# Kernel optimization log

Measured on AMD Instinct MI355X. Metric: run time of the kernel, lower is better.

## Reference

```python
import jax, jax.numpy as jnp
import numpy as np

N_NODES = 100000


def _glorot(key, shape):
    fan_in, fan_out = shape[1], shape[0]
    lim = np.sqrt(6.0 / (fan_in + fan_out))
    return jax.random.uniform(key, shape, jnp.float32, -lim, lim)


def setup_inputs() -> dict:
    key = jax.random.key(0)
    ks = jax.random.split(key, 12)
    x = jax.random.normal(ks[0], (N_NODES, 64), jnp.float32)
    edge_index = jax.random.randint(ks[1], (2, 1600000), 0, N_NODES, jnp.int64)
    return {
        "x": x,
        "edge_index": edge_index,
        # SAGEConv layer 1: lin_l (neighbors, with bias), lin_r (root, no bias)
        "W1l": _glorot(ks[2], (64, 64)), "b1": jnp.zeros((64,), jnp.float32), "W1r": _glorot(ks[3], (64, 64)),
        "W2l": _glorot(ks[4], (64, 64)), "b2": jnp.zeros((64,), jnp.float32), "W2r": _glorot(ks[5], (64, 64)),
        "W3l": _glorot(ks[6], (32, 64)), "b3": jnp.zeros((32,), jnp.float32), "W3r": _glorot(ks[7], (32, 64)),
        "Wreg": _glorot(ks[8], (1, 32)), "breg": jnp.zeros((1,), jnp.float32),
    }


def _sage_conv(x, src, dst, Wl, b, Wr):
    # mean aggregation of source-node features at destination nodes
    msg_sum = jax.ops.segment_sum(x[src], dst, num_segments=N_NODES)  # [N, d]
    deg = jax.ops.segment_sum(jnp.ones_like(src, dtype=x.dtype), dst, num_segments=N_NODES)
    mean = msg_sum / jnp.maximum(deg, 1.0)[:, None]
    return mean @ Wl.T + b + x @ Wr.T


def reference(x, edge_index, W1l, b1, W1r, W2l, b2, W2r, W3l, b3, W3r, Wreg, breg):
    src, dst = edge_index[0], edge_index[1]
    h = jax.nn.relu(_sage_conv(x, src, dst, W1l, b1, W1r))
    h = jax.nn.relu(_sage_conv(h, src, dst, W2l, b2, W2r))
    h = jax.nn.relu(_sage_conv(h, src, dst, W3l, b3, W3r))
    return (h @ Wreg.T + breg).squeeze(-1)  # [N]
```

## Files before the change

kernel.cpp:

```cpp
#include <hip/hip_runtime.h>
#include <math.h>

#define N_NODES 100000
#define N_EDGES 1600000
#define NB 782
#define NTILES 6250
#define NPART 256

typedef unsigned int uint;
typedef __attribute__((ext_vector_type(8))) short bf16x8;
typedef __attribute__((ext_vector_type(4))) float f32x4;

__device__ inline ushort f2bf(float f) {
    uint u = __float_as_uint(f);
    uint r = (u + 0x7fffu + ((u >> 16) & 1u)) >> 16;
    return (ushort)r;
}
__device__ inline uint pack2bf(float lo, float hi) {
    return (uint)f2bf(lo) | ((uint)f2bf(hi) << 16);
}

__global__ void misc_kernel(const float* __restrict__ W1l, const float* __restrict__ W1r,
                            const float* __restrict__ W2l, const float* __restrict__ W2r,
                            const float* __restrict__ W3l, const float* __restrict__ W3r,
                            ushort* __restrict__ wf,
                            const float* __restrict__ x, ushort* __restrict__ xb) {
    if (blockIdx.x < 80) {
        int idx = blockIdx.x * 256 + threadIdx.x;
        if (idx >= 20480) return;
        const float *Wl, *Wr;
        int base, KT;
        if (idx < 8192)       { base = 0;     Wl = W1l; Wr = W1r; KT = 128; }
        else if (idx < 16384) { base = 8192;  Wl = W2l; Wr = W2r; KT = 128; }
        else if (idx < 18432) { base = 16384; Wl = W3l; Wr = 0;   KT = 64; }
        else                  { base = 18432; Wl = W3r; Wr = 0;   KT = 64; }
        int r = idx - base;
        int f = r >> 9;
        int l = (r >> 3) & 63;
        int i = r & 7;
        int nks = KT >> 5;
        int nt = f / nks, ks = f - nt * nks;
        int k = ks * 32 + ((l >> 4) << 3) + i;
        int j = nt * 16 + (l & 15);
        float v = (k < 64) ? Wl[j * 64 + k] : Wr[j * 64 + (k - 64)];
        wf[idx] = f2bf(v);
    } else {
        const int n4 = N_NODES * 64 / 4;
        int i0 = (blockIdx.x - 80) * 256 + threadIdx.x;
        for (int i = i0; i < n4; i += 400 * 256) {
            float4 v = ((const float4*)x)[i];
            uint2 o;
            o.x = pack2bf(v.x, v.y);
            o.y = pack2bf(v.z, v.w);
            ((uint2*)xb)[i] = o;
        }
    }
}

__global__ void bucket_hist(const int* __restrict__ dst, int* __restrict__ hist2D, int nE) {
    __shared__ int hist[NB];
    const int PER = (N_EDGES + NPART - 1) / NPART;
    int e0 = blockIdx.x * PER;
    int e1 = min(e0 + PER, nE);
    for (int i = threadIdx.x; i < NB; i += 1024) hist[i] = 0;
    __syncthreads();
    for (int e = e0 + threadIdx.x; e < e1; e += 1024)
        atomicAdd(&hist[dst[e] >> 7], 1);
    __syncthreads();
    for (int i = threadIdx.x; i < NB; i += 1024)
        hist2D[blockIdx.x * NB + i] = hist[i];
}

__global__ void scan_buckets(const int* __restrict__ hist2D, int* __restrict__ bucketBase,
                             int* __restrict__ base2D) {
    __shared__ int s[1024];
    int tid = threadIdx.x;
    int tot = 0;
    if (tid < NB)
        for (int b = 0; b < NPART; ++b) tot += hist2D[b * NB + tid];
    s[tid] = tot;
    __syncthreads();
    for (int off = 1; off < 1024; off <<= 1) {
        int t = (tid >= off) ? s[tid - off] : 0;
        __syncthreads();
        s[tid] += t;
        __syncthreads();
    }
    if (tid < NB) {
        int run = s[tid] - tot;
        bucketBase[tid] = run;
        for (int b = 0; b < NPART; ++b) {
            base2D[b * NB + tid] = run;
            run += hist2D[b * NB + tid];
        }
    }
    if (tid == 0) bucketBase[NB] = s[NB - 1];
}

__global__ void partition_kernel(const int* __restrict__ src, const int* __restrict__ dst,
                                 const int* __restrict__ base2D, int* __restrict__ part, int nE) {
    __shared__ int base[NB];
    __shared__ int rank[NB];
    const int PER = (N_EDGES + NPART - 1) / NPART;
    int e0 = blockIdx.x * PER;
    int e1 = min(e0 + PER, nE);
    for (int i = threadIdx.x; i < NB; i += 1024) {
        base[i] = base2D[blockIdx.x * NB + i];
        rank[i] = 0;
    }
    __syncthreads();
    for (int e = e0 + threadIdx.x; e < e1; e += 1024) {
        int d = dst[e];
        int bk = d >> 7;
        int r = atomicAdd(&rank[bk], 1);
        part[base[bk] + r] = src[e] | ((d & 127) << 20);
    }
}

__global__ void bucket_fill2(const int* __restrict__ bucketBase, const int* __restrict__ part,
                             int* __restrict__ col, int* __restrict__ rowptr,
                             float* __restrict__ invdeg, int n) {
    __shared__ int cnt[128];
    __shared__ int cnt2[128];
    __shared__ int exclS[128];
    __shared__ int s[128];
    int b = blockIdx.x;
    int d0 = b << 7;
    int dl = min(128, n - d0);
    int ebeg = bucketBase[b], eend = bucketBase[b + 1];
    if (threadIdx.x < 128) { cnt[threadIdx.x] = 0; cnt2[threadIdx.x] = 0; }
    __syncthreads();
    for (int i = ebeg + (int)threadIdx.x; i < eend; i += 512)
        atomicAdd(&cnt[part[i] >> 20], 1);
    __syncthreads();
    if (threadIdx.x < 128) s[threadIdx.x] = cnt[threadIdx.x];
    __syncthreads();
    for (int off = 1; off < 128; off <<= 1) {
        int t = 0;
        if (threadIdx.x < 128 && threadIdx.x >= (unsigned)off) t = s[threadIdx.x - off];
        __syncthreads();
        if (threadIdx.x < 128) s[threadIdx.x] += t;
        __syncthreads();
    }
    if ((int)threadIdx.x < dl) {
        int c = cnt[threadIdx.x];
        int ex = ebeg + s[threadIdx.x] - c;
        rowptr[d0 + threadIdx.x] = ex;
        invdeg[d0 + threadIdx.x] = 1.0f / fmaxf((float)c, 1.0f);
        exclS[threadIdx.x] = ex;
    }
    if (threadIdx.x == 0 && d0 + dl == n) rowptr[n] = eend;
    __syncthreads();
    for (int i = ebeg + (int)threadIdx.x; i < eend; i += 512) {
        int v = part[i];
        int doff = v >> 20;
        int pos = exclS[doff] + atomicAdd(&cnt2[doff], 1);
        col[pos] = v & 0xFFFFF;
    }
}

__global__ void gather_mean(const ushort* __restrict__ xb, const int* __restrict__ rowptr,
                            const int* __restrict__ col, const float* __restrict__ invdeg,
                            ushort* __restrict__ meanb, int n) {
    int tid = blockIdx.x * blockDim.x + threadIdx.x;
    int wid = tid >> 6;
    int lane = threadIdx.x & 63;
    int grp = lane >> 3;
    int li = lane & 7;
    int node = wid * 8 + grp;
    if (node >= n) return;
    int beg = rowptr[node];
    int end = rowptr[node + 1];
    int fb = li * 8;
    float a0 = 0.f, a1 = 0.f, a2 = 0.f, a3 = 0.f, a4 = 0.f, a5 = 0.f, a6 = 0.f, a7 = 0.f;
    for (int i = beg; i < end; i += 8) {
        int idx = i + li;
        int ci = (idx < end) ? col[idx] : 0;
        int cnt = end - i;
#pragma unroll
        for (int t = 0; t < 8; ++t) {
            if (t < cnt) {
                int s = __shfl(ci, grp * 8 + t, 64);
                uint4 w = *(const uint4*)(xb + (size_t)s * 64 + fb);
                a0 += __uint_as_float(w.x << 16);
                a1 += __uint_as_float(w.x & 0xffff0000u);
                a2 += __uint_as_float(w.y << 16);
                a3 += __uint_as_float(w.y & 0xffff0000u);
                a4 += __uint_as_float(w.z << 16);
                a5 += __uint_as_float(w.z & 0xffff0000u);
                a6 += __uint_as_float(w.w << 16);
                a7 += __uint_as_float(w.w & 0xffff0000u);
            }
        }
    }
    float id = invdeg[node];
    uint4 o;
    o.x = pack2bf(a0 * id, a1 * id);
    o.y = pack2bf(a2 * id, a3 * id);
    o.z = pack2bf(a4 * id, a5 * id);
    o.w = pack2bf(a6 * id, a7 * id);
    *(uint4*)(meanb + (size_t)node * 64 + fb) = o;
}

__global__ void gather_mean32(const ushort* __restrict__ gb, const int* __restrict__ rowptr,
                              const int* __restrict__ col, const float* __restrict__ invdeg,
                              ushort* __restrict__ mean32b, int n) {
    int tid = blockIdx.x * blockDim.x + threadIdx.x;
    int wid = tid >> 6;
    int lane = threadIdx.x & 63;
    int grp = lane >> 2;
    int li = lane & 3;
    int node = wid * 16 + grp;
    if (node >= n) return;
    int beg = rowptr[node];
    int end = rowptr[node + 1];
    int fb = li * 8;
    float a0 = 0.f, a1 = 0.f, a2 = 0.f, a3 = 0.f, a4 = 0.f, a5 = 0.f, a6 = 0.f, a7 = 0.f;
    for (int i = beg; i < end; i += 4) {
        int idx = i + li;
        int ci = (idx < end) ? col[idx] : 0;
        int cnt = end - i;
#pragma unroll
        for (int t = 0; t < 4; ++t) {
            if (t < cnt) {
                int s = __shfl(ci, grp * 4 + t, 64);
                uint4 w = *(const uint4*)(gb + (size_t)s * 32 + fb);
                a0 += __uint_as_float(w.x << 16);
                a1 += __uint_as_float(w.x & 0xffff0000u);
                a2 += __uint_as_float(w.y << 16);
                a3 += __uint_as_float(w.y & 0xffff0000u);
                a4 += __uint_as_float(w.z << 16);
                a5 += __uint_as_float(w.z & 0xffff0000u);
                a6 += __uint_as_float(w.w << 16);
                a7 += __uint_as_float(w.w & 0xffff0000u);
            }
        }
    }
    float id = invdeg[node];
    uint4 o;
    o.x = pack2bf(a0 * id, a1 * id);
    o.y = pack2bf(a2 * id, a3 * id);
    o.z = pack2bf(a4 * id, a5 * id);
    o.w = pack2bf(a6 * id, a7 * id);
    *(uint4*)(mean32b + (size_t)node * 32 + fb) = o;
}

__global__ void __launch_bounds__(256)
mfma_transform(const ushort* __restrict__ rootb, const ushort* __restrict__ meanb,
               const ushort* __restrict__ wfrag, const float* __restrict__ bias,
               ushort* __restrict__ outb, int ntiles) {
    int wave = threadIdx.x >> 6;
    int lane = threadIdx.x & 63;

    bf16x8 wf[4][4];
#pragma unroll
    for (int nt = 0; nt < 4; ++nt)
#pragma unroll
        for (int ks = 0; ks < 4; ++ks)
            wf[nt][ks] = *(const bf16x8*)(wfrag + (size_t)((nt * 4 + ks) * 64 + lane) * 8);

    float bl[4];
#pragma unroll
    for (int nt = 0; nt < 4; ++nt) bl[nt] = bias[nt * 16 + (lane & 15)];

    int arow = lane & 15;
    int koff = (lane >> 4) * 8;
    int crow = (lane >> 4) * 4;
    int nwaves = gridDim.x * 4;

    for (int tile = blockIdx.x * 4 + wave; tile < ntiles; tile += nwaves) {
        int n0 = tile * 16;
        const ushort* mrow = meanb + (size_t)(n0 + arow) * 64 + koff;
        const ushort* xrow = rootb + (size_t)(n0 + arow) * 64 + koff;
        bf16x8 a0 = *(const bf16x8*)(mrow);
        bf16x8 a1 = *(const bf16x8*)(mrow + 32);
        bf16x8 a2 = *(const bf16x8*)(xrow);
        bf16x8 a3 = *(const bf16x8*)(xrow + 32);
#pragma unroll
        for (int nt = 0; nt < 4; ++nt) {
            f32x4 c = {0.f, 0.f, 0.f, 0.f};
            c = __builtin_amdgcn_mfma_f32_16x16x32_bf16(a0, wf[nt][0], c, 0, 0, 0);
            c = __builtin_amdgcn_mfma_f32_16x16x32_bf16(a1, wf[nt][1], c, 0, 0, 0);
            c = __builtin_amdgcn_mfma_f32_16x16x32_bf16(a2, wf[nt][2], c, 0, 0, 0);
            c = __builtin_amdgcn_mfma_f32_16x16x32_bf16(a3, wf[nt][3], c, 0, 0, 0);
#pragma unroll
            for (int i = 0; i < 4; ++i) {
                float v = fmaxf(c[i] + bl[nt], 0.0f);
                outb[(size_t)(n0 + crow + i) * 64 + nt * 16 + (lane & 15)] = f2bf(v);
            }
        }
    }
}

__global__ void __launch_bounds__(256)
mfma_pretrans3(const ushort* __restrict__ hb, const ushort* __restrict__ wfrag,
               ushort* __restrict__ gb, int ntiles) {
    int wave = threadIdx.x >> 6;
    int lane = threadIdx.x & 63;

    bf16x8 wf[2][2];
#pragma unroll
    for (int nt = 0; nt < 2; ++nt)
#pragma unroll
        for (int ks = 0; ks < 2; ++ks)
            wf[nt][ks] = *(const bf16x8*)(wfrag + (size_t)((nt * 2 + ks) * 64 + lane) * 8);

    int arow = lane & 15;
    int koff = (lane >> 4) * 8;
    int crow = (lane >> 4) * 4;
    int nwaves = gridDim.x * 4;

    for (int tile = blockIdx.x * 4 + wave; tile < ntiles; tile += nwaves) {
        int n0 = tile * 16;
        const ushort* hrow = hb + (size_t)(n0 + arow) * 64 + koff;
        bf16x8 a0 = *(const bf16x8*)(hrow);
        bf16x8 a1 = *(const bf16x8*)(hrow + 32);
#pragma unroll
        for (int nt = 0; nt < 2; ++nt) {
            f32x4 c = {0.f, 0.f, 0.f, 0.f};
            c = __builtin_amdgcn_mfma_f32_16x16x32_bf16(a0, wf[nt][0], c, 0, 0, 0);
            c = __builtin_amdgcn_mfma_f32_16x16x32_bf16(a1, wf[nt][1], c, 0, 0, 0);
#pragma unroll
            for (int i = 0; i < 4; ++i)
                gb[(size_t)(n0 + crow + i) * 32 + nt * 16 + (lane & 15)] = f2bf(c[i]);
        }
    }
}

__global__ void __launch_bounds__(256)
mfma_t3(const ushort* __restrict__ hb, const ushort* __restrict__ mean32b,
        const ushort* __restrict__ wfrag, const float* __restrict__ b3,
        const float* __restrict__ Wreg, const float* __restrict__ breg,
        float* __restrict__ out, int ntiles) {
    int wave = threadIdx.x >> 6;
    int lane = threadIdx.x & 63;

    bf16x8 wf[2][2];
#pragma unroll
    for (int nt = 0; nt < 2; ++nt)
#pragma unroll
        for (int ks = 0; ks < 2; ++ks)
            wf[nt][ks] = *(const bf16x8*)(wfrag + (size_t)((nt * 2 + ks) * 64 + lane) * 8);

    float bl[2], wr[2];
#pragma unroll
    for (int nt = 0; nt < 2; ++nt) {
        bl[nt] = b3[nt * 16 + (lane & 15)];
        wr[nt] = Wreg[nt * 16 + (lane & 15)];
    }
    float br = breg[0];

    int arow = lane & 15;
    int koff = (lane >> 4) * 8;
    int crow = (lane >> 4) * 4;
    int nwaves = gridDim.x * 4;

    for (int tile = blockIdx.x * 4 + wave; tile < ntiles; tile += nwaves) {
        int n0 = tile * 16;
        const ushort* hrow = hb + (size_t)(n0 + arow) * 64 + koff;
        bf16x8 a0 = *(const bf16x8*)(hrow);
        bf16x8 a1 = *(const bf16x8*)(hrow + 32);
        float part0 = 0.f, part1 = 0.f, part2 = 0.f, part3 = 0.f;
#pragma unroll
        for (int nt = 0; nt < 2; ++nt) {
            f32x4 c = {0.f, 0.f, 0.f, 0.f};
            c = __builtin_amdgcn_mfma_f32_16x16x32_bf16(a0, wf[nt][0], c, 0, 0, 0);
            c = __builtin_amdgcn_mfma_f32_16x16x32_bf16(a1, wf[nt][1], c, 0, 0, 0);
#pragma unroll
            for (int i = 0; i < 4; ++i) {
                ushort mw = mean32b[(size_t)(n0 + crow + i) * 32 + nt * 16 + (lane & 15)];
                float m = __uint_as_float((uint)mw << 16);
                float v = fmaxf(c[i] + bl[nt] + m, 0.0f) * wr[nt];
                if (i == 0) part0 += v;
                else if (i == 1) part1 += v;
                else if (i == 2) part2 += v;
                else part3 += v;
            }
        }
#pragma unroll
        for (int s = 1; s < 16; s <<= 1) {
            part0 += __shfl_xor(part0, s, 64);
            part1 += __shfl_xor(part1, s, 64);
            part2 += __shfl_xor(part2, s, 64);
            part3 += __shfl_xor(part3, s, 64);
        }
        if ((lane & 15) == 0) {
            float4 o;
            o.x = part0 + br; o.y = part1 + br; o.z = part2 + br; o.w = part3 + br;
            *(float4*)(out + n0 + crow) = o;
        }
    }
}

extern "C" void kernel_launch(void* const* d_in, const int* in_sizes, int n_in,
                              void* d_out, int out_size, void* d_ws, size_t ws_size,
                              hipStream_t stream) {
    const float* x    = (const float*)d_in[0];
    const int*   ei   = (const int*)d_in[1];
    const float* W1l  = (const float*)d_in[2];
    const float* b1   = (const float*)d_in[3];
    const float* W1r  = (const float*)d_in[4];
    const float* W2l  = (const float*)d_in[5];
    const float* b2   = (const float*)d_in[6];
    const float* W2r  = (const float*)d_in[7];
    const float* W3l  = (const float*)d_in[8];
    const float* b3   = (const float*)d_in[9];
    const float* W3r  = (const float*)d_in[10];
    const float* Wreg = (const float*)d_in[11];
    const float* breg = (const float*)d_in[12];

    const int* src = ei;
    const int* dst = ei + N_EDGES;

    char* p = (char*)d_ws;
    auto alloc = [&](size_t bytes) {
        char* r = p;
        p += (bytes + 255) & ~(size_t)255;
        return r;
    };
    int*    hist2D    = (int*)alloc((size_t)NPART * NB * sizeof(int));
    int*    base2D    = (int*)alloc((size_t)NPART * NB * sizeof(int));
    int*    bucketBase= (int*)alloc((NB + 1) * sizeof(int));
    int*    rowptr    = (int*)alloc((N_NODES + 1) * sizeof(int));
    int*    col       = (int*)alloc((size_t)N_EDGES * sizeof(int));
    float*  invdeg    = (float*)alloc(N_NODES * sizeof(float));
    ushort* wfrag     = (ushort*)alloc(20480 * sizeof(ushort));
    char*   slot   = (char*)alloc((size_t)N_EDGES * sizeof(int));
    int*    part   = (int*)slot;
    ushort* gb     = (ushort*)slot;
    ushort* xb     = (ushort*)alloc((size_t)N_NODES * 64 * sizeof(ushort));
    ushort* meanb  = (ushort*)alloc((size_t)N_NODES * 64 * sizeof(ushort));
    ushort* mean32b= meanb;
    ushort* hb     = (ushort*)alloc((size_t)N_NODES * 64 * sizeof(ushort));
    float*  out    = (float*)d_out;

    const int TB = 256;
    int g64Blocks    = (N_NODES * 8 + TB - 1) / TB;
    int g32Blocks    = (N_NODES * 4 + TB - 1) / TB;
    const int mfmaBlocks = 1563;

    misc_kernel<<<480, 256, 0, stream>>>(W1l, W1r, W2l, W2r, W3l, W3r, wfrag, x, xb);
    bucket_hist<<<NPART, 1024, 0, stream>>>(dst, hist2D, N_EDGES);
    scan_buckets<<<1, 1024, 0, stream>>>(hist2D, bucketBase, base2D);
    partition_kernel<<<NPART, 1024, 0, stream>>>(src, dst, base2D, part, N_EDGES);
    bucket_fill2<<<NB, 512, 0, stream>>>(bucketBase, part, col, rowptr, invdeg, N_NODES);

    gather_mean<<<g64Blocks, 256, 0, stream>>>(xb, rowptr, col, invdeg, meanb, N_NODES);
    mfma_transform<<<mfmaBlocks, 256, 0, stream>>>(xb, meanb, wfrag + 0, b1, hb, NTILES);

    gather_mean<<<g64Blocks, 256, 0, stream>>>(hb, rowptr, col, invdeg, meanb, N_NODES);
    mfma_transform<<<mfmaBlocks, 256, 0, stream>>>(hb, meanb, wfrag + 8192, b2, hb, NTILES);

    mfma_pretrans3<<<mfmaBlocks, 256, 0, stream>>>(hb, wfrag + 16384, gb, NTILES);
    gather_mean32<<<g32Blocks, 256, 0, stream>>>(gb, rowptr, col, invdeg, mean32b, N_NODES);
    mfma_t3<<<mfmaBlocks, 256, 0, stream>>>(hb, mean32b, wfrag + 18432, b3, Wreg, breg, out, NTILES);
}
```

Baseline: 196.8 us.

## Parallelize bucket offset scan across blocks and shrink MFMA grid

```diff
diff --git a/kernel.cpp b/kernel.cpp
--- a/kernel.cpp
+++ b/kernel.cpp
@@ -71,14 +71,28 @@
         hist2D[blockIdx.x * NB + i] = hist[i];
 }
 
-__global__ void scan_buckets(const int* __restrict__ hist2D, int* __restrict__ bucketBase,
-                             int* __restrict__ base2D) {
+__global__ void col_scan(const int* __restrict__ hist2D, int* __restrict__ colExcl,
+                         int* __restrict__ bucketTot) {
+    __shared__ int s[NPART];
+    int i = blockIdx.x;
+    int v = hist2D[threadIdx.x * NB + i];
+    s[threadIdx.x] = v;
+    __syncthreads();
+    for (int off = 1; off < NPART; off <<= 1) {
+        int t = (threadIdx.x >= (unsigned)off) ? s[threadIdx.x - off] : 0;
+        __syncthreads();
+        s[threadIdx.x] += t;
+        __syncthreads();
+    }
+    colExcl[threadIdx.x * NB + i] = s[threadIdx.x] - v;
+    if (threadIdx.x == NPART - 1) bucketTot[i] = s[NPART - 1];
+}
+
+__global__ void scan_tot(const int* __restrict__ bucketTot, int* __restrict__ bucketBase) {
     __shared__ int s[1024];
     int tid = threadIdx.x;
-    int tot = 0;
-    if (tid < NB)
-        for (int b = 0; b < NPART; ++b) tot += hist2D[b * NB + tid];
-    s[tid] = tot;
+    int v = (tid < NB) ? bucketTot[tid] : 0;
+    s[tid] = v;
     __syncthreads();
     for (int off = 1; off < 1024; off <<= 1) {
         int t = (tid >= off) ? s[tid - off] : 0;
@@ -86,26 +100,20 @@
         s[tid] += t;
         __syncthreads();
     }
-    if (tid < NB) {
-        int run = s[tid] - tot;
-        bucketBase[tid] = run;
-        for (int b = 0; b < NPART; ++b) {
-            base2D[b * NB + tid] = run;
-            run += hist2D[b * NB + tid];
-        }
-    }
+    if (tid < NB) bucketBase[tid] = s[tid] - v;
     if (tid == 0) bucketBase[NB] = s[NB - 1];
 }
 
 __global__ void partition_kernel(const int* __restrict__ src, const int* __restrict__ dst,
-                                 const int* __restrict__ base2D, int* __restrict__ part, int nE) {
+                                 const int* __restrict__ bucketBase, const int* __restrict__ colExcl,
+                                 int* __restrict__ part, int nE) {
     __shared__ int base[NB];
     __shared__ int rank[NB];
     const int PER = (N_EDGES + NPART - 1) / NPART;
     int e0 = blockIdx.x * PER;
     int e1 = min(e0 + PER, nE);
     for (int i = threadIdx.x; i < NB; i += 1024) {
-        base[i] = base2D[blockIdx.x * NB + i];
+        base[i] = bucketBase[i] + colExcl[blockIdx.x * NB + i];
         rank[i] = 0;
     }
     __syncthreads();
@@ -419,7 +427,8 @@
         return r;
     };
     int*    hist2D    = (int*)alloc((size_t)NPART * NB * sizeof(int));
-    int*    base2D    = (int*)alloc((size_t)NPART * NB * sizeof(int));
+    int*    colExcl   = (int*)alloc((size_t)NPART * NB * sizeof(int));
+    int*    bucketTot = (int*)alloc(NB * sizeof(int));
     int*    bucketBase= (int*)alloc((NB + 1) * sizeof(int));
     int*    rowptr    = (int*)alloc((N_NODES + 1) * sizeof(int));
     int*    col       = (int*)alloc((size_t)N_EDGES * sizeof(int));
@@ -437,12 +446,13 @@
     const int TB = 256;
     int g64Blocks    = (N_NODES * 8 + TB - 1) / TB;
     int g32Blocks    = (N_NODES * 4 + TB - 1) / TB;
-    const int mfmaBlocks = 1563;
+    const int mfmaBlocks = 512;
 
     misc_kernel<<<480, 256, 0, stream>>>(W1l, W1r, W2l, W2r, W3l, W3r, wfrag, x, xb);
     bucket_hist<<<NPART, 1024, 0, stream>>>(dst, hist2D, N_EDGES);
-    scan_buckets<<<1, 1024, 0, stream>>>(hist2D, bucketBase, base2D);
-    partition_kernel<<<NPART, 1024, 0, stream>>>(src, dst, base2D, part, N_EDGES);
+    col_scan<<<NB, NPART, 0, stream>>>(hist2D, colExcl, bucketTot);
+    scan_tot<<<1, 1024, 0, stream>>>(bucketTot, bucketBase);
+    partition_kernel<<<NPART, 1024, 0, stream>>>(src, dst, bucketBase, colExcl, part, N_EDGES);
     bucket_fill2<<<NB, 512, 0, stream>>>(bucketBase, part, col, rowptr, invdeg, N_NODES);
 
     gather_mean<<<g64Blocks, 256, 0, stream>>>(xb, rowptr, col, invdeg, meanb, N_NODES);
```

Result: faster. 169.0 us (-14.1%).
